# Kernel optimization log

Hardware: AMD Instinct MI355X
Metric: run time of the kernel (lower is better)

## Reference

```python
import jax, jax.numpy as jnp
import numpy as np

B, N, F, E, U, V = 64, 64, 512, 512, 1024, 32000  # batch, num_feature_vectors, feat_dim, embed_dim, units, vocab


def setup_inputs() -> dict:
    key = jax.random.key(0)
    ks = jax.random.split(key, 16)
    s = 0.05  # tf.random_normal_initializer default stddev
    return {
        "y": jax.random.randint(ks[0], (B, 1), 0, V),
        "features": jax.random.normal(ks[1], (B, N, F), jnp.float32),
        "state_output": jax.random.normal(ks[2], (B, U), jnp.float32),
        "h": jax.random.normal(ks[3], (B, U), jnp.float32),
        "c": jax.random.normal(ks[4], (B, U), jnp.float32),
        "Q": jax.random.normal(ks[5], (U, U), jnp.float32) * s,
        "K": jax.random.normal(ks[6], (U, N), jnp.float32) * s,
        "emb": jax.random.normal(ks[7], (V, E), jnp.float32) * 0.02,
        "W_x": jax.random.normal(ks[8], (F + E, 4 * U), jnp.float32) * 0.02,
        "W_h": jax.random.normal(ks[9], (U, 4 * U), jnp.float32) * 0.02,
        "b_lstm": jnp.zeros((4 * U,), jnp.float32),
        "W1": jax.random.normal(ks[10], (U, U), jnp.float32) * 0.02,
        "b1": jnp.zeros((U,), jnp.float32),
        "W2": jax.random.normal(ks[11], (U, V), jnp.float32) * 0.02,
        "b2": jnp.zeros((V,), jnp.float32),
    }


def reference(y, features, state_output, h, c, Q, K, emb, W_x, W_h, b_lstm, W1, b1, W2, b2):
    # DotProductAttention: per-example loop collapsed into one batched einsum.
    # w[b, n] = ((Q @ state^T)^T @ K)[b, n]  (same for every example i)
    w = (Q @ state_output.T).T @ K                      # [B, N]
    # loop body: aw[i] = w @ features[i]  -> stacked [B(i), B(b), F]
    aw = jnp.einsum('bn,inf->ibf', w, features)         # [B, B, F]
    aw = jax.nn.softmax(aw, axis=-1)                    # tf.nn.softmax default axis=-1
    context = jnp.sum(aw * features, axis=1)            # [B, F] (requires N == B)

    ye = emb[y[:, 0]]                                   # embedding + squeeze(axis=1): [B, E]
    x = jnp.concatenate([context, ye], axis=-1)         # [B, F+E]

    # Keras LSTMCell (gate order i, f, g, o)
    z = x @ W_x + h @ W_h + b_lstm                      # [B, 4U]
    zi, zf, zg, zo = jnp.split(z, 4, axis=-1)
    i_g = jax.nn.sigmoid(zi)
    f_g = jax.nn.sigmoid(zf)
    g_g = jnp.tanh(zg)
    o_g = jax.nn.sigmoid(zo)
    c_new = f_g * c + i_g * g_g
    h_new = o_g * jnp.tanh(c_new)

    logits = (h_new @ W1 + b1) @ W2 + b2                # fc1 (linear) -> fc2: [B, V]
    return logits, h_new, (h_new, c_new), aw
```

## Files before the change

### kernel.cpp

```cpp
#include <hip/hip_runtime.h>
#include <math.h>

#define WS_S    0
#define WS_W    65536
#define WS_CTX  69632
#define WS_YE   102400
#define WS_Z    135168
#define WS_T1   397312

#define OUT_LOGITS 0
#define OUT_H1     2048000
#define OUT_H2     2113536
#define OUT_C      2179072
#define OUT_AW     2244608

#define FMA4(ACC, A, W) { ACC.x += (A)*(W).x; ACC.y += (A)*(W).y; \
                          ACC.z += (A)*(W).z; ACC.w += (A)*(W).w; }

#define FMA16(WV, A0, A1, A2, A3) { \
    FMA4(acc[0],  A0.x, WV) FMA4(acc[1],  A0.y, WV) \
    FMA4(acc[2],  A0.z, WV) FMA4(acc[3],  A0.w, WV) \
    FMA4(acc[4],  A1.x, WV) FMA4(acc[5],  A1.y, WV) \
    FMA4(acc[6],  A1.z, WV) FMA4(acc[7],  A1.w, WV) \
    FMA4(acc[8],  A2.x, WV) FMA4(acc[9],  A2.y, WV) \
    FMA4(acc[10], A2.z, WV) FMA4(acc[11], A2.w, WV) \
    FMA4(acc[12], A3.x, WV) FMA4(acc[13], A3.y, WV) \
    FMA4(acc[14], A3.z, WV) FMA4(acc[15], A3.w, WV) }

__global__ __launch_bounds__(256) void k0_init(const int* __restrict__ y,
    const float* __restrict__ emb, const float* __restrict__ b_lstm,
    const float* __restrict__ b1, float* __restrict__ ws) {
  int idx = blockIdx.x * 256 + threadIdx.x;
  ws[WS_S + idx] = 0.f;
  ws[WS_T1 + idx] = b1[idx & 1023];
  *reinterpret_cast<float4*>(&ws[WS_Z + idx * 4]) =
      *reinterpret_cast<const float4*>(&b_lstm[(idx * 4) & 4095]);
  if (idx < 36864) ws[WS_W + idx] = 0.f;
  if (idx < 32768) {
    int b = idx >> 9, e = idx & 511;
    ws[WS_YE + idx] = emb[(size_t)y[b] * 512 + e];
  }
}

__global__ __launch_bounds__(256) void kb2_init(const float* __restrict__ b2,
    float* __restrict__ out) {
  int n = blockIdx.x * 256 + threadIdx.x;
  int r0 = blockIdx.y * 16;
  float v = b2[n];
  float* p = out + OUT_LOGITS + (size_t)r0 * 32000 + n;
#pragma unroll
  for (int r = 0; r < 16; ++r) p[(size_t)r * 32000] = v;
}

__global__ __launch_bounds__(256) void k1_sgemm(const float* __restrict__ so,
    const float* __restrict__ Q, float* __restrict__ ws) {
  __shared__ float Qt[64][65];
  __shared__ float SOt[64][68];
  int u0 = blockIdx.x * 64;
  int k0 = blockIdx.y * 64;
  int tid = threadIdx.x;
  for (int i = 0; i < 16; ++i) {
    int idx = tid + i * 256;
    int r = idx >> 6, k_l = idx & 63;
    Qt[k_l][r]  = Q[(u0 + r) * 1024 + k0 + k_l];
    SOt[k_l][r] = so[r * 1024 + k0 + k_l];
  }
  __syncthreads();
  int u = tid & 63, g = tid >> 6;
  float acc[16];
#pragma unroll
  for (int j = 0; j < 16; ++j) acc[j] = 0.f;
  for (int k_l = 0; k_l < 64; ++k_l) {
    float qv = Qt[k_l][u];
    const float4* sp = reinterpret_cast<const float4*>(&SOt[k_l][g * 16]);
    float4 s0 = sp[0], s1 = sp[1], s2 = sp[2], s3 = sp[3];
    acc[0]  += s0.x * qv; acc[1]  += s0.y * qv; acc[2]  += s0.z * qv; acc[3]  += s0.w * qv;
    acc[4]  += s1.x * qv; acc[5]  += s1.y * qv; acc[6]  += s1.z * qv; acc[7]  += s1.w * qv;
    acc[8]  += s2.x * qv; acc[9]  += s2.y * qv; acc[10] += s2.z * qv; acc[11] += s2.w * qv;
    acc[12] += s3.x * qv; acc[13] += s3.y * qv; acc[14] += s3.z * qv; acc[15] += s3.w * qv;
  }
  float* s_out = ws + WS_S;
#pragma unroll
  for (int j = 0; j < 16; ++j)
    atomicAdd(&s_out[(g * 16 + j) * 1024 + u0 + u], acc[j]);
}

__global__ __launch_bounds__(256) void k2_wgemm(const float* __restrict__ Katt,
    float* __restrict__ ws) {
  __shared__ float St[64][68];
  __shared__ float Kl[64][65];
  int k0 = blockIdx.x * 64;
  int tid = threadIdx.x;
  const float* s_in = ws + WS_S;
  for (int i = 0; i < 16; ++i) {
    int idx = tid + i * 256;
    int r = idx >> 6, q = idx & 63;
    St[q][r] = s_in[r * 1024 + k0 + q];
    Kl[r][q] = Katt[(k0 + r) * 64 + q];
  }
  __syncthreads();
  int n = tid & 63, g = tid >> 6;
  float acc[16];
#pragma unroll
  for (int j = 0; j < 16; ++j) acc[j] = 0.f;
  for (int k_l = 0; k_l < 64; ++k_l) {
    float kv = Kl[k_l][n];
    const float4* sp = reinterpret_cast<const float4*>(&St[k_l][g * 16]);
    float4 s0 = sp[0], s1 = sp[1], s2 = sp[2], s3 = sp[3];
    acc[0]  += s0.x * kv; acc[1]  += s0.y * kv; acc[2]  += s0.z * kv; acc[3]  += s0.w * kv;
    acc[4]  += s1.x * kv; acc[5]  += s1.y * kv; acc[6]  += s1.z * kv; acc[7]  += s1.w * kv;
    acc[8]  += s2.x * kv; acc[9]  += s2.y * kv; acc[10] += s2.z * kv; acc[11] += s2.w * kv;
    acc[12] += s3.x * kv; acc[13] += s3.y * kv; acc[14] += s3.z * kv; acc[15] += s3.w * kv;
  }
  float* w_out = ws + WS_W;
#pragma unroll
  for (int j = 0; j < 16; ++j)
    atomicAdd(&w_out[(g * 16 + j) * 64 + n], acc[j]);
}

__global__ __launch_bounds__(256) void k3_attn(const float* __restrict__ feat,
    float* __restrict__ ws, float* __restrict__ out) {
  __shared__ float wt[64][8];
  __shared__ float red[32];
  int i = blockIdx.x;
  int b0 = blockIdx.y * 8;
  int tid = threadIdx.x;
  int lane = tid & 63, wid = tid >> 6;
  const float* w_g = ws + WS_W;
  for (int t = tid; t < 512; t += 256) {
    int j = t >> 6, n = t & 63;
    wt[n][j] = w_g[(b0 + j) * 64 + n];
  }
  __syncthreads();
  const float* fi = feat + i * 32768;
  int f0 = tid * 2;
  float2 sc[8];
#pragma unroll
  for (int j = 0; j < 8; ++j) sc[j] = make_float2(0.f, 0.f);
  for (int n = 0; n < 64; n += 8) {
    float2 fv[8];
#pragma unroll
    for (int t = 0; t < 8; ++t)
      fv[t] = *reinterpret_cast<const float2*>(&fi[(n + t) * 512 + f0]);
#pragma unroll
    for (int t = 0; t < 8; ++t) {
      const float4* wp = reinterpret_cast<const float4*>(&wt[n + t][0]);
      float4 w0 = wp[0], w1 = wp[1];
      sc[0].x += w0.x * fv[t].x; sc[0].y += w0.x * fv[t].y;
      sc[1].x += w0.y * fv[t].x; sc[1].y += w0.y * fv[t].y;
      sc[2].x += w0.z * fv[t].x; sc[2].y += w0.z * fv[t].y;
      sc[3].x += w0.w * fv[t].x; sc[3].y += w0.w * fv[t].y;
      sc[4].x += w1.x * fv[t].x; sc[4].y += w1.x * fv[t].y;
      sc[5].x += w1.y * fv[t].x; sc[5].y += w1.y * fv[t].y;
      sc[6].x += w1.z * fv[t].x; sc[6].y += w1.z * fv[t].y;
      sc[7].x += w1.w * fv[t].x; sc[7].y += w1.w * fv[t].y;
    }
  }
  float m[8];
#pragma unroll
  for (int j = 0; j < 8; ++j) m[j] = fmaxf(sc[j].x, sc[j].y);
  for (int d = 1; d < 64; d <<= 1) {
#pragma unroll
    for (int j = 0; j < 8; ++j) m[j] = fmaxf(m[j], __shfl_xor(m[j], d));
  }
  if (lane == 0) {
#pragma unroll
    for (int j = 0; j < 8; ++j) red[wid * 8 + j] = m[j];
  }
  __syncthreads();
#pragma unroll
  for (int j = 0; j < 8; ++j)
    m[j] = fmaxf(fmaxf(red[j], red[8 + j]), fmaxf(red[16 + j], red[24 + j]));
  __syncthreads();
  float sm[8];
#pragma unroll
  for (int j = 0; j < 8; ++j) {
    sc[j].x = __expf(sc[j].x - m[j]);
    sc[j].y = __expf(sc[j].y - m[j]);
    sm[j] = sc[j].x + sc[j].y;
  }
  for (int d = 1; d < 64; d <<= 1) {
#pragma unroll
    for (int j = 0; j < 8; ++j) sm[j] += __shfl_xor(sm[j], d);
  }
  if (lane == 0) {
#pragma unroll
    for (int j = 0; j < 8; ++j) red[wid * 8 + j] = sm[j];
  }
  __syncthreads();
#pragma unroll
  for (int j = 0; j < 8; ++j)
    sm[j] = (red[j] + red[8 + j]) + (red[16 + j] + red[24 + j]);
  float2 ctx = make_float2(0.f, 0.f);
#pragma unroll
  for (int j = 0; j < 8; ++j) {
    float is = 1.f / sm[j];
    float ax = sc[j].x * is, ay = sc[j].y * is;
    *reinterpret_cast<float2*>(&out[OUT_AW + (i * 64 + b0 + j) * 512 + f0]) =
        make_float2(ax, ay);
    float2 fb = *reinterpret_cast<const float2*>(&fi[(b0 + j) * 512 + f0]);
    ctx.x += ax * fb.x;
    ctx.y += ay * fb.y;
  }
  float* ctxp = ws + WS_CTX + i * 512 + f0;
  atomicAdd(&ctxp[0], ctx.x);
  atomicAdd(&ctxp[1], ctx.y);
}

__global__ __launch_bounds__(256) void k5_zgemm(const float* __restrict__ h,
    const float* __restrict__ Wx, const float* __restrict__ Wh,
    float* __restrict__ ws) {
  __shared__ float At[128][68];
  int n0 = blockIdx.x * 256;
  int kc = blockIdx.y * 128;
  int tid = threadIdx.x;
  int lane = tid & 63, r0 = (tid >> 6) * 16;
  const float* src; int stride; int koff;
  if (kc < 512)       { src = ws + WS_CTX; stride = 512;  koff = kc; }
  else if (kc < 1024) { src = ws + WS_YE;  stride = 512;  koff = kc - 512; }
  else                { src = h;           stride = 1024; koff = kc - 1024; }
  for (int it = 0; it < 32; ++it) {
    int idx = tid + it * 256;
    int k_l = idx & 127, b = idx >> 7;
    At[k_l][b] = src[b * stride + koff + k_l];
  }
  __syncthreads();
  const float* wp = ((kc < 1024) ? (Wx + (size_t)kc * 4096)
                                 : (Wh + (size_t)(kc - 1024) * 4096))
                    + n0 + lane * 4;
  float4 acc[16];
#pragma unroll
  for (int j = 0; j < 16; ++j) acc[j] = make_float4(0.f, 0.f, 0.f, 0.f);
  float4 wv0[8], wv1[8];
#pragma unroll
  for (int t = 0; t < 8; ++t)
    wv0[t] = *reinterpret_cast<const float4*>(wp + (size_t)t * 4096);
  for (int kb = 0; kb < 128; kb += 16) {
#pragma unroll
    for (int t = 0; t < 8; ++t)
      wv1[t] = *reinterpret_cast<const float4*>(wp + (size_t)(kb + 8 + t) * 4096);
#pragma unroll
    for (int t = 0; t < 8; ++t) {
      const float4* ap = reinterpret_cast<const float4*>(&At[kb + t][r0]);
      float4 a0 = ap[0], a1 = ap[1], a2 = ap[2], a3 = ap[3];
      FMA16(wv0[t], a0, a1, a2, a3)
    }
    if (kb + 16 < 128) {
#pragma unroll
      for (int t = 0; t < 8; ++t)
        wv0[t] = *reinterpret_cast<const float4*>(wp + (size_t)(kb + 16 + t) * 4096);
    }
#pragma unroll
    for (int t = 0; t < 8; ++t) {
      const float4* ap = reinterpret_cast<const float4*>(&At[kb + 8 + t][r0]);
      float4 a0 = ap[0], a1 = ap[1], a2 = ap[2], a3 = ap[3];
      FMA16(wv1[t], a0, a1, a2, a3)
    }
  }
  float* zp = ws + WS_Z + (size_t)r0 * 4096 + n0 + lane * 4;
#pragma unroll
  for (int j = 0; j < 16; ++j) {
    atomicAdd(&zp[(size_t)j * 4096 + 0], acc[j].x);
    atomicAdd(&zp[(size_t)j * 4096 + 1], acc[j].y);
    atomicAdd(&zp[(size_t)j * 4096 + 2], acc[j].z);
    atomicAdd(&zp[(size_t)j * 4096 + 3], acc[j].w);
  }
}

__global__ __launch_bounds__(256) void k6_gates(const float* __restrict__ ws,
    const float* __restrict__ c, float* __restrict__ out) {
  int idx = blockIdx.x * 256 + threadIdx.x;
  int b = idx >> 10, u = idx & 1023;
  const float* z = ws + WS_Z;
  float zi = z[b * 4096 + u];
  float zf = z[b * 4096 + 1024 + u];
  float zg = z[b * 4096 + 2048 + u];
  float zo = z[b * 4096 + 3072 + u];
  float ig = 1.f / (1.f + __expf(-zi));
  float fg = 1.f / (1.f + __expf(-zf));
  float gg = tanhf(zg);
  float og = 1.f / (1.f + __expf(-zo));
  float cn = fg * c[idx] + ig * gg;
  float hn = og * tanhf(cn);
  out[OUT_H1 + idx] = hn;
  out[OUT_H2 + idx] = hn;
  out[OUT_C + idx] = cn;
}

__global__ __launch_bounds__(256) void k7_t1gemm(const float* __restrict__ out_r,
    const float* __restrict__ W1, float* __restrict__ ws) {
  __shared__ float At[64][68];
  int n0 = blockIdx.x * 64;
  int k0 = blockIdx.y * 64;
  int tid = threadIdx.x;
  const float* hn = out_r + OUT_H1;
  for (int it = 0; it < 16; ++it) {
    int idx = tid + it * 256;
    int k_l = idx & 63, b = idx >> 6;
    At[k_l][b] = hn[b * 1024 + k0 + k_l];
  }
  __syncthreads();
  int ng = tid & 15, g = tid >> 4;
  const float* wp = W1 + (size_t)k0 * 1024 + n0 + ng * 4;
  float4 acc[4];
#pragma unroll
  for (int j = 0; j < 4; ++j) acc[j] = make_float4(0.f, 0.f, 0.f, 0.f);
  for (int kb = 0; kb < 64; kb += 8) {
    float4 wv[8];
#pragma unroll
    for (int t = 0; t < 8; ++t)
      wv[t] = *reinterpret_cast<const float4*>(wp + (size_t)(kb + t) * 1024);
#pragma unroll
    for (int t = 0; t < 8; ++t) {
      float4 a0 = *reinterpret_cast<const float4*>(&At[kb + t][g * 4]);
      FMA4(acc[0], a0.x, wv[t]) FMA4(acc[1], a0.y, wv[t])
      FMA4(acc[2], a0.z, wv[t]) FMA4(acc[3], a0.w, wv[t])
    }
  }
  float* t1 = ws + WS_T1 + (size_t)(g * 4) * 1024 + n0 + ng * 4;
#pragma unroll
  for (int j = 0; j < 4; ++j) {
    atomicAdd(&t1[(size_t)j * 1024 + 0], acc[j].x);
    atomicAdd(&t1[(size_t)j * 1024 + 1], acc[j].y);
    atomicAdd(&t1[(size_t)j * 1024 + 2], acc[j].z);
    atomicAdd(&t1[(size_t)j * 1024 + 3], acc[j].w);
  }
}

__global__ __launch_bounds__(256) void k8_logits(const float* __restrict__ W2,
    const float* __restrict__ wsr, float* __restrict__ out) {
  __shared__ float At[128][68];
  int n0 = blockIdx.x * 256;
  int k0b = blockIdx.y * 256;
  int tid = threadIdx.x;
  int lane = tid & 63, r0 = (tid >> 6) * 16;
  const float* t1 = wsr + WS_T1;
  float4 acc[16];
#pragma unroll
  for (int j = 0; j < 16; ++j) acc[j] = make_float4(0.f, 0.f, 0.f, 0.f);
  for (int s = 0; s < 2; ++s) {
    int kc = k0b + s * 128;
    if (s) __syncthreads();
    for (int it = 0; it < 32; ++it) {
      int idx = tid + it * 256;
      int k_l = idx & 127, b = idx >> 7;
      At[k_l][b] = t1[b * 1024 + kc + k_l];
    }
    __syncthreads();
    const float* wp = W2 + (size_t)kc * 32000 + n0 + lane * 4;
    float4 wv0[8], wv1[8];
#pragma unroll
    for (int t = 0; t < 8; ++t)
      wv0[t] = *reinterpret_cast<const float4*>(wp + (size_t)t * 32000);
    for (int kb = 0; kb < 128; kb += 16) {
#pragma unroll
      for (int t = 0; t < 8; ++t)
        wv1[t] = *reinterpret_cast<const float4*>(wp + (size_t)(kb + 8 + t) * 32000);
#pragma unroll
      for (int t = 0; t < 8; ++t) {
        const float4* ap = reinterpret_cast<const float4*>(&At[kb + t][r0]);
        float4 a0 = ap[0], a1 = ap[1], a2 = ap[2], a3 = ap[3];
        FMA16(wv0[t], a0, a1, a2, a3)
      }
      if (kb + 16 < 128) {
#pragma unroll
        for (int t = 0; t < 8; ++t)
          wv0[t] = *reinterpret_cast<const float4*>(wp + (size_t)(kb + 16 + t) * 32000);
      }
#pragma unroll
      for (int t = 0; t < 8; ++t) {
        const float4* ap = reinterpret_cast<const float4*>(&At[kb + 8 + t][r0]);
        float4 a0 = ap[0], a1 = ap[1], a2 = ap[2], a3 = ap[3];
        FMA16(wv1[t], a0, a1, a2, a3)
      }
    }
  }
  float* op = out + OUT_LOGITS + (size_t)r0 * 32000 + n0 + lane * 4;
#pragma unroll
  for (int j = 0; j < 16; ++j) {
    atomicAdd(&op[(size_t)j * 32000 + 0], acc[j].x);
    atomicAdd(&op[(size_t)j * 32000 + 1], acc[j].y);
    atomicAdd(&op[(size_t)j * 32000 + 2], acc[j].z);
    atomicAdd(&op[(size_t)j * 32000 + 3], acc[j].w);
  }
}

extern "C" void kernel_launch(void* const* d_in, const int* in_sizes, int n_in,
                              void* d_out, int out_size, void* d_ws, size_t ws_size,
                              hipStream_t stream) {
  const int*   y    = (const int*)  d_in[0];
  const float* feat = (const float*)d_in[1];
  const float* so   = (const float*)d_in[2];
  const float* h    = (const float*)d_in[3];
  const float* c    = (const float*)d_in[4];
  const float* Q    = (const float*)d_in[5];
  const float* Katt = (const float*)d_in[6];
  const float* emb  = (const float*)d_in[7];
  const float* Wx   = (const float*)d_in[8];
  const float* Wh   = (const float*)d_in[9];
  const float* bl   = (const float*)d_in[10];
  const float* W1   = (const float*)d_in[11];
  const float* b1   = (const float*)d_in[12];
  const float* W2   = (const float*)d_in[13];
  const float* b2   = (const float*)d_in[14];
  float* ws  = (float*)d_ws;
  float* out = (float*)d_out;

  k0_init  <<<256, 256, 0, stream>>>(y, emb, bl, b1, ws);
  kb2_init <<<dim3(125, 4), 256, 0, stream>>>(b2, out);
  k1_sgemm <<<dim3(16, 16), 256, 0, stream>>>(so, Q, ws);
  k2_wgemm <<<16, 256, 0, stream>>>(Katt, ws);
  k3_attn  <<<dim3(64, 8), 256, 0, stream>>>(feat, ws, out);
  k5_zgemm <<<dim3(16, 16), 256, 0, stream>>>(h, Wx, Wh, ws);
  k6_gates <<<256, 256, 0, stream>>>(ws, c, out);
  k7_t1gemm<<<dim3(16, 16), 256, 0, stream>>>(out, W1, ws);
  k8_logits<<<dim3(125, 4), 256, 0, stream>>>(W2, ws, out);
}
```

Before: 511.2 us.

## Remove split-K atomics in logits GEMM, transpose activations, fold bias inits

The logits GEMM now runs the full K=1024 inside each block over narrower 64-column tiles, split among four k-groups inside the wave and reduced with shuffles. Results are written with plain float4 stores plus b2 bias, which removes the b2 init kernel and the heavy atomic traffic on the 8 MB logits output. Activations (x concatenation and t1) are stored transposed in the workspace so the shared-memory tile loads become coalesced float4 reads. The z GEMM gets the same intra-block k-group tiling, and bias init is moved into the gates kernel. In exchange, each logits block now does a longer serial K loop and the grid has fewer blocks.

Result: faster. 409.7 us (-19.8%).

```diff
diff --git a/kernel.cpp b/kernel.cpp
--- a/kernel.cpp
+++ b/kernel.cpp
@@ -2,11 +2,10 @@
 #include <math.h>
 
 #define WS_S    0
+#define WS_T1T  0
 #define WS_W    65536
-#define WS_CTX  69632
-#define WS_YE   102400
-#define WS_Z    135168
-#define WS_T1   397312
+#define WS_XT   69632
+#define WS_Z    200704
 
 #define OUT_LOGITS 0
 #define OUT_H1     2048000
@@ -29,27 +28,18 @@
 
 __global__ __launch_bounds__(256) void k0_init(const int* __restrict__ y,
     const float* __restrict__ emb, const float* __restrict__ b_lstm,
-    const float* __restrict__ b1, float* __restrict__ ws) {
+    const float* __restrict__ h, float* __restrict__ ws) {
   int idx = blockIdx.x * 256 + threadIdx.x;
   ws[WS_S + idx] = 0.f;
-  ws[WS_T1 + idx] = b1[idx & 1023];
   *reinterpret_cast<float4*>(&ws[WS_Z + idx * 4]) =
       *reinterpret_cast<const float4*>(&b_lstm[(idx * 4) & 4095]);
-  if (idx < 36864) ws[WS_W + idx] = 0.f;
+  ws[WS_XT + (size_t)(1024 + (idx & 1023)) * 64 + (idx >> 10)] = h[idx];
   if (idx < 32768) {
+    ws[WS_XT + idx] = 0.f;
     int b = idx >> 9, e = idx & 511;
-    ws[WS_YE + idx] = emb[(size_t)y[b] * 512 + e];
-  }
-}
-
-__global__ __launch_bounds__(256) void kb2_init(const float* __restrict__ b2,
-    float* __restrict__ out) {
-  int n = blockIdx.x * 256 + threadIdx.x;
-  int r0 = blockIdx.y * 16;
-  float v = b2[n];
-  float* p = out + OUT_LOGITS + (size_t)r0 * 32000 + n;
-#pragma unroll
-  for (int r = 0; r < 16; ++r) p[(size_t)r * 32000] = v;
+    ws[WS_XT + (size_t)(512 + e) * 64 + b] = emb[(size_t)y[b] * 512 + e];
+  }
+  if (idx < 4096) ws[WS_W + idx] = 0.f;
 }
 
 __global__ __launch_bounds__(256) void k1_sgemm(const float* __restrict__ so,
@@ -196,79 +186,89 @@
   for (int j = 0; j < 8; ++j) {
     float is = 1.f / sm[j];
     float ax = sc[j].x * is, ay = sc[j].y * is;
-    *reinterpret_cast<float2*>(&out[OUT_AW + (i * 64 + b0 + j) * 512 + f0]) =
+    *reinterpret_cast<float2*>(&out[OUT_AW + (size_t)(i * 64 + b0 + j) * 512 + f0]) =
         make_float2(ax, ay);
     float2 fb = *reinterpret_cast<const float2*>(&fi[(b0 + j) * 512 + f0]);
     ctx.x += ax * fb.x;
     ctx.y += ay * fb.y;
   }
-  float* ctxp = ws + WS_CTX + i * 512 + f0;
-  atomicAdd(&ctxp[0], ctx.x);
-  atomicAdd(&ctxp[1], ctx.y);
-}
-
-__global__ __launch_bounds__(256) void k5_zgemm(const float* __restrict__ h,
-    const float* __restrict__ Wx, const float* __restrict__ Wh,
-    float* __restrict__ ws) {
+  atomicAdd(&ws[WS_XT + (size_t)f0 * 64 + i], ctx.x);
+  atomicAdd(&ws[WS_XT + (size_t)(f0 + 1) * 64 + i], ctx.y);
+}
+
+__global__ __launch_bounds__(256) void k5_zgemm(const float* __restrict__ Wx,
+    const float* __restrict__ Wh, float* __restrict__ ws) {
   __shared__ float At[128][68];
-  int n0 = blockIdx.x * 256;
-  int kc = blockIdx.y * 128;
+  int n0 = blockIdx.x * 64;
+  int kbase = blockIdx.y * 256;
   int tid = threadIdx.x;
   int lane = tid & 63, r0 = (tid >> 6) * 16;
-  const float* src; int stride; int koff;
-  if (kc < 512)       { src = ws + WS_CTX; stride = 512;  koff = kc; }
-  else if (kc < 1024) { src = ws + WS_YE;  stride = 512;  koff = kc - 512; }
-  else                { src = h;           stride = 1024; koff = kc - 1024; }
-  for (int it = 0; it < 32; ++it) {
-    int idx = tid + it * 256;
-    int k_l = idx & 127, b = idx >> 7;
-    At[k_l][b] = src[b * stride + koff + k_l];
-  }
-  __syncthreads();
-  const float* wp = ((kc < 1024) ? (Wx + (size_t)kc * 4096)
-                                 : (Wh + (size_t)(kc - 1024) * 4096))
-                    + n0 + lane * 4;
+  int kg = lane >> 4, c4 = (lane & 15) * 4;
+  const float* xT = ws + WS_XT;
   float4 acc[16];
 #pragma unroll
   for (int j = 0; j < 16; ++j) acc[j] = make_float4(0.f, 0.f, 0.f, 0.f);
-  float4 wv0[8], wv1[8];
-#pragma unroll
-  for (int t = 0; t < 8; ++t)
-    wv0[t] = *reinterpret_cast<const float4*>(wp + (size_t)t * 4096);
-  for (int kb = 0; kb < 128; kb += 16) {
+  for (int s = 0; s < 2; ++s) {
+    int kc = kbase + s * 128;
+    if (s) __syncthreads();
+    for (int it = 0; it < 8; ++it) {
+      int idx = tid + it * 256;
+      int k_l = idx >> 4, f4 = (idx & 15) * 4;
+      float4 v = *reinterpret_cast<const float4*>(xT + (size_t)(kc + k_l) * 64 + f4);
+      *reinterpret_cast<float4*>(&At[k_l][f4]) = v;
+    }
+    __syncthreads();
+    const float* wp = ((kc < 1024) ? (Wx + (size_t)kc * 4096)
+                                   : (Wh + (size_t)(kc - 1024) * 4096))
+                      + (size_t)kg * 4096 + n0 + c4;
+    float4 wv0[8], wv1[8];
 #pragma unroll
     for (int t = 0; t < 8; ++t)
-      wv1[t] = *reinterpret_cast<const float4*>(wp + (size_t)(kb + 8 + t) * 4096);
-#pragma unroll
-    for (int t = 0; t < 8; ++t) {
-      const float4* ap = reinterpret_cast<const float4*>(&At[kb + t][r0]);
-      float4 a0 = ap[0], a1 = ap[1], a2 = ap[2], a3 = ap[3];
-      FMA16(wv0[t], a0, a1, a2, a3)
-    }
-    if (kb + 16 < 128) {
+      wv0[t] = *reinterpret_cast<const float4*>(wp + (size_t)(t * 4) * 4096);
+    for (int kb = 0; kb < 32; kb += 16) {
 #pragma unroll
       for (int t = 0; t < 8; ++t)
-        wv0[t] = *reinterpret_cast<const float4*>(wp + (size_t)(kb + 16 + t) * 4096);
-    }
-#pragma unroll
-    for (int t = 0; t < 8; ++t) {
-      const float4* ap = reinterpret_cast<const float4*>(&At[kb + 8 + t][r0]);
-      float4 a0 = ap[0], a1 = ap[1], a2 = ap[2], a3 = ap[3];
-      FMA16(wv1[t], a0, a1, a2, a3)
-    }
-  }
-  float* zp = ws + WS_Z + (size_t)r0 * 4096 + n0 + lane * 4;
+        wv1[t] = *reinterpret_cast<const float4*>(wp + (size_t)((kb + 8 + t) * 4) * 4096);
+#pragma unroll
+      for (int t = 0; t < 8; ++t) {
+        const float4* ap = reinterpret_cast<const float4*>(&At[(kb + t) * 4 + kg][r0]);
+        float4 a0 = ap[0], a1 = ap[1], a2 = ap[2], a3 = ap[3];
+        FMA16(wv0[t], a0, a1, a2, a3)
+      }
+      if (kb + 16 < 32) {
+#pragma unroll
+        for (int t = 0; t < 8; ++t)
+          wv0[t] = *reinterpret_cast<const float4*>(wp + (size_t)((kb + 16 + t) * 4) * 4096);
+      }
+#pragma unroll
+      for (int t = 0; t < 8; ++t) {
+        const float4* ap = reinterpret_cast<const float4*>(&At[(kb + 8 + t) * 4 + kg][r0]);
+        float4 a0 = ap[0], a1 = ap[1], a2 = ap[2], a3 = ap[3];
+        FMA16(wv1[t], a0, a1, a2, a3)
+      }
+    }
+  }
 #pragma unroll
   for (int j = 0; j < 16; ++j) {
-    atomicAdd(&zp[(size_t)j * 4096 + 0], acc[j].x);
-    atomicAdd(&zp[(size_t)j * 4096 + 1], acc[j].y);
-    atomicAdd(&zp[(size_t)j * 4096 + 2], acc[j].z);
-    atomicAdd(&zp[(size_t)j * 4096 + 3], acc[j].w);
-  }
-}
-
-__global__ __launch_bounds__(256) void k6_gates(const float* __restrict__ ws,
-    const float* __restrict__ c, float* __restrict__ out) {
+    acc[j].x += __shfl_xor(acc[j].x, 16); acc[j].y += __shfl_xor(acc[j].y, 16);
+    acc[j].z += __shfl_xor(acc[j].z, 16); acc[j].w += __shfl_xor(acc[j].w, 16);
+    acc[j].x += __shfl_xor(acc[j].x, 32); acc[j].y += __shfl_xor(acc[j].y, 32);
+    acc[j].z += __shfl_xor(acc[j].z, 32); acc[j].w += __shfl_xor(acc[j].w, 32);
+  }
+  float* zb = ws + WS_Z + n0 + c4;
+#define ZST(J, RR) { float* p = zb + (size_t)(r0 + RR) * 4096; \
+    atomicAdd(p, acc[J].x); atomicAdd(p + 1, acc[J].y); \
+    atomicAdd(p + 2, acc[J].z); atomicAdd(p + 3, acc[J].w); }
+  if (kg == 0)      { ZST(0, 0)  ZST(1, 1)  ZST(2, 2)   ZST(3, 3) }
+  else if (kg == 1) { ZST(4, 4)  ZST(5, 5)  ZST(6, 6)   ZST(7, 7) }
+  else if (kg == 2) { ZST(8, 8)  ZST(9, 9)  ZST(10, 10) ZST(11, 11) }
+  else              { ZST(12, 12) ZST(13, 13) ZST(14, 14) ZST(15, 15) }
+#undef ZST
+}
+
+__global__ __launch_bounds__(256) void k6_gates(float* __restrict__ ws,
+    const float* __restrict__ c, const float* __restrict__ b1,
+    float* __restrict__ out) {
   int idx = blockIdx.x * 256 + threadIdx.x;
   int b = idx >> 10, u = idx & 1023;
   const float* z = ws + WS_Z;
@@ -285,6 +285,7 @@
   out[OUT_H1 + idx] = hn;
   out[OUT_H2 + idx] = hn;
   out[OUT_C + idx] = cn;
+  ws[WS_T1T + idx] = b1[idx >> 6];
 }
 
 __global__ __launch_bounds__(256) void k7_t1gemm(const float* __restrict__ out_r,
@@ -317,72 +318,84 @@
       FMA4(acc[2], a0.z, wv[t]) FMA4(acc[3], a0.w, wv[t])
     }
   }
-  float* t1 = ws + WS_T1 + (size_t)(g * 4) * 1024 + n0 + ng * 4;
+  float* t1T = ws + WS_T1T;
 #pragma unroll
   for (int j = 0; j < 4; ++j) {
-    atomicAdd(&t1[(size_t)j * 1024 + 0], acc[j].x);
-    atomicAdd(&t1[(size_t)j * 1024 + 1], acc[j].y);
-    atomicAdd(&t1[(size_t)j * 1024 + 2], acc[j].z);
-    atomicAdd(&t1[(size_t)j * 1024 + 3], acc[j].w);
+    int b = g * 4 + j;
+    atomicAdd(&t1T[(size_t)(n0 + ng * 4 + 0) * 64 + b], acc[j].x);
+    atomicAdd(&t1T[(size_t)(n0 + ng * 4 + 1) * 64 + b], acc[j].y);
+    atomicAdd(&t1T[(size_t)(n0 + ng * 4 + 2) * 64 + b], acc[j].z);
+    atomicAdd(&t1T[(size_t)(n0 + ng * 4 + 3) * 64 + b], acc[j].w);
   }
 }
 
 __global__ __launch_bounds__(256) void k8_logits(const float* __restrict__ W2,
-    const float* __restrict__ wsr, float* __restrict__ out) {
+    const float* __restrict__ b2, const float* __restrict__ wsr,
+    float* __restrict__ out) {
   __shared__ float At[128][68];
-  int n0 = blockIdx.x * 256;
-  int k0b = blockIdx.y * 256;
+  int n0 = blockIdx.x * 64;
   int tid = threadIdx.x;
   int lane = tid & 63, r0 = (tid >> 6) * 16;
-  const float* t1 = wsr + WS_T1;
+  int kg = lane >> 4, c4 = (lane & 15) * 4;
+  const float* t1T = wsr + WS_T1T;
+  float4 bias = *reinterpret_cast<const float4*>(b2 + n0 + c4);
+  const float* wbase = W2 + (size_t)kg * 32000 + n0 + c4;
   float4 acc[16];
 #pragma unroll
   for (int j = 0; j < 16; ++j) acc[j] = make_float4(0.f, 0.f, 0.f, 0.f);
-  for (int s = 0; s < 2; ++s) {
-    int kc = k0b + s * 128;
-    if (s) __syncthreads();
-    for (int it = 0; it < 32; ++it) {
+  for (int kc = 0; kc < 1024; kc += 128) {
+    if (kc) __syncthreads();
+    for (int it = 0; it < 8; ++it) {
       int idx = tid + it * 256;
-      int k_l = idx & 127, b = idx >> 7;
-      At[k_l][b] = t1[b * 1024 + kc + k_l];
+      int k_l = idx >> 4, f4 = (idx & 15) * 4;
+      float4 v = *reinterpret_cast<const float4*>(t1T + (size_t)(kc + k_l) * 64 + f4);
+      *reinterpret_cast<float4*>(&At[k_l][f4]) = v;
     }
     __syncthreads();
-    const float* wp = W2 + (size_t)kc * 32000 + n0 + lane * 4;
+    const float* wp = wbase + (size_t)kc * 32000;
     float4 wv0[8], wv1[8];
 #pragma unroll
     for (int t = 0; t < 8; ++t)
-      wv0[t] = *reinterpret_cast<const float4*>(wp + (size_t)t * 32000);
-    for (int kb = 0; kb < 128; kb += 16) {
+      wv0[t] = *reinterpret_cast<const float4*>(wp + (size_t)(t * 4) * 32000);
+    for (int kb = 0; kb < 32; kb += 16) {
 #pragma unroll
       for (int t = 0; t < 8; ++t)
-        wv1[t] = *reinterpret_cast<const float4*>(wp + (size_t)(kb + 8 + t) * 32000);
+        wv1[t] = *reinterpret_cast<const float4*>(wp + (size_t)((kb + 8 + t) * 4) * 32000);
 #pragma unroll
       for (int t = 0; t < 8; ++t) {
-        const float4* ap = reinterpret_cast<const float4*>(&At[kb + t][r0]);
+        const float4* ap = reinterpret_cast<const float4*>(&At[(kb + t) * 4 + kg][r0]);
         float4 a0 = ap[0], a1 = ap[1], a2 = ap[2], a3 = ap[3];
         FMA16(wv0[t], a0, a1, a2, a3)
       }
-      if (kb + 16 < 128) {
+      if (kb + 16 < 32) {
 #pragma unroll
         for (int t = 0; t < 8; ++t)
-          wv0[t] = *reinterpret_cast<const float4*>(wp + (size_t)(kb + 16 + t) * 32000);
+          wv0[t] = *reinterpret_cast<const float4*>(wp + (size_t)((kb + 16 + t) * 4) * 32000);
       }
 #pragma unroll
       for (int t = 0; t < 8; ++t) {
-        const float4* ap = reinterpret_cast<const float4*>(&At[kb + 8 + t][r0]);
+        const float4* ap = reinterpret_cast<const float4*>(&At[(kb + 8 + t) * 4 + kg][r0]);
         float4 a0 = ap[0], a1 = ap[1], a2 = ap[2], a3 = ap[3];
         FMA16(wv1[t], a0, a1, a2, a3)
       }
     }
   }
-  float* op = out + OUT_LOGITS + (size_t)r0 * 32000 + n0 + lane * 4;
 #pragma unroll
   for (int j = 0; j < 16; ++j) {
-    atomicAdd(&op[(size_t)j * 32000 + 0], acc[j].x);
-    atomicAdd(&op[(size_t)j * 32000 + 1], acc[j].y);
-    atomicAdd(&op[(size_t)j * 32000 + 2], acc[j].z);
-    atomicAdd(&op[(size_t)j * 32000 + 3], acc[j].w);
-  }
+    acc[j].x += __shfl_xor(acc[j].x, 16); acc[j].y += __shfl_xor(acc[j].y, 16);
+    acc[j].z += __shfl_xor(acc[j].z, 16); acc[j].w += __shfl_xor(acc[j].w, 16);
+    acc[j].x += __shfl_xor(acc[j].x, 32); acc[j].y += __shfl_xor(acc[j].y, 32);
+    acc[j].z += __shfl_xor(acc[j].z, 32); acc[j].w += __shfl_xor(acc[j].w, 32);
+  }
+  float* ob = out + OUT_LOGITS + n0 + c4;
+#define LST(J, RR) { float4 v = acc[J]; \
+    v.x += bias.x; v.y += bias.y; v.z += bias.z; v.w += bias.w; \
+    *reinterpret_cast<float4*>(ob + (size_t)(r0 + RR) * 32000) = v; }
+  if (kg == 0)      { LST(0, 0)   LST(1, 1)   LST(2, 2)   LST(3, 3) }
+  else if (kg == 1) { LST(4, 4)   LST(5, 5)   LST(6, 6)   LST(7, 7) }
+  else if (kg == 2) { LST(8, 8)   LST(9, 9)   LST(10, 10) LST(11, 11) }
+  else              { LST(12, 12) LST(13, 13) LST(14, 14) LST(15, 15) }
+#undef LST
 }
 
 extern "C" void kernel_launch(void* const* d_in, const int* in_sizes, int n_in,
@@ -406,13 +419,12 @@
   float* ws  = (float*)d_ws;
   float* out = (float*)d_out;
 
-  k0_init  <<<256, 256, 0, stream>>>(y, emb, bl, b1, ws);
-  kb2_init <<<dim3(125, 4), 256, 0, stream>>>(b2, out);
+  k0_init  <<<256, 256, 0, stream>>>(y, emb, bl, h, ws);
   k1_sgemm <<<dim3(16, 16), 256, 0, stream>>>(so, Q, ws);
   k2_wgemm <<<16, 256, 0, stream>>>(Katt, ws);
   k3_attn  <<<dim3(64, 8), 256, 0, stream>>>(feat, ws, out);
-  k5_zgemm <<<dim3(16, 16), 256, 0, stream>>>(h, Wx, Wh, ws);
-  k6_gates <<<256, 256, 0, stream>>>(ws, c, out);
+  k5_zgemm <<<dim3(64, 8), 256, 0, stream>>>(Wx, Wh, ws);
+  k6_gates <<<256, 256, 0, stream>>>(ws, c, b1, out);
   k7_t1gemm<<<dim3(16, 16), 256, 0, stream>>>(out, W1, ws);
-  k8_logits<<<dim3(125, 4), 256, 0, stream>>>(W2, ws, out);
-}
+  k8_logits<<<500, 256, 0, stream>>>(W2, b2, ws, out);
+}
```
